# Optimization experiments

Measured on AMD Instinct MI355X. Metric: run time of the kernel, lower is better.

The kernel has to match this reference:

```python
import jax, jax.numpy as jnp
import numpy as np

KS = 3
K2 = KS * KS
PAD = 1


def conv2d(x, w, b=None, stride=1, pad=0):
    out = jax.lax.conv_general_dilated(
        x, w, (stride, stride), [(pad, pad), (pad, pad)],
        dimension_numbers=("NCHW", "OIHW", "NCHW"))
    if b is not None:
        out = out + b[None, :, None, None]
    return out


def setup_inputs() -> dict:
    key = jax.random.key(0)
    ks = jax.random.split(key, 11)
    B, C, H, W = 4, 64, 128, 128
    s = 0.05  # weight scale keeps offsets in a sane range
    return {
        "x":      jax.random.normal(ks[0], (B, C, H, W), jnp.float32),
        "ref":    jax.random.normal(ks[1], (B, C, H, W), jnp.float32),
        "w_cd":   jax.random.normal(ks[2], (C, 2 * C, 1, 1), jnp.float32) * s,
        "b_cd":   jax.random.normal(ks[3], (C,), jnp.float32) * s,
        "w_p":    jax.random.normal(ks[4], (2 * K2, C, 3, 3), jnp.float32) * s,
        "b_p":    jax.random.normal(ks[5], (2 * K2,), jnp.float32) * s,
        "w_m":    jax.random.normal(ks[6], (K2, C, 3, 3), jnp.float32) * s,
        "b_m":    jax.random.normal(ks[7], (K2,), jnp.float32) * s,
        "w_c":    jax.random.normal(ks[8], (K2 * C, C, 3, 3), jnp.float32) * s,
        "b_c":    jax.random.normal(ks[9], (K2 * C,), jnp.float32) * s,
        "w_conv": jax.random.normal(ks[10], (C, C, 3, 3), jnp.float32) * s,
    }


def _deform_forward(x, ref, w_cd, b_cd, w_p, b_p, w_m, b_m, w_c, b_c, w_conv):
    B, C, H, W = x.shape
    dt = x.dtype

    # offset / modulation / color nets on fused input
    fused = conv2d(jnp.concatenate([x, ref], axis=1), w_cd, b_cd)          # [B,C,H,W]
    off = conv2d(fused, w_p, b_p, pad=1)                                    # [B,2K2,H,W]
    mod = jax.nn.sigmoid(conv2d(fused, w_m, b_m, pad=1))                    # [B,K2,H,W]
    col = jnp.tanh(conv2d(fused, w_c, b_c, pad=1))                          # [B,K2*C,H,W]

    # zero-pad input; sampling grid carries the +padding shift (arange starts at 1)
    xp = jnp.pad(x, ((0, 0), (0, 0), (PAD, PAD), (PAD, PAD)))
    Hp, Wp = H + 2 * PAD, W + 2 * PAD

    gx = jnp.broadcast_to(jnp.arange(1, H + 1, dtype=dt)[:, None], (H, W))
    gy = jnp.broadcast_to(jnp.arange(1, W + 1, dtype=dt)[None, :], (H, W))
    r = (KS - 1) // 2
    cx, cy = jnp.meshgrid(jnp.arange(-r, r + 1, dtype=dt),
                          jnp.arange(-r, r + 1, dtype=dt), indexing="ij")
    px = gx[None, None] + off[:, :K2] + cx.ravel()[None, :, None, None]     # [B,K2,H,W]
    py = gy[None, None] + off[:, K2:] + cy.ravel()[None, :, None, None]

    # integer neighbors (detached, like torch .detach().floor())
    fx = jax.lax.stop_gradient(jnp.floor(px))
    fy = jax.lax.stop_gradient(jnp.floor(py))
    q_ltx = jnp.clip(fx, 0, Hp - 1); q_lty = jnp.clip(fy, 0, Wp - 1)
    q_rbx = jnp.clip(fx + 1, 0, Hp - 1); q_rby = jnp.clip(fy + 1, 0, Wp - 1)

    # clamped sampling locations for weights
    sx = jnp.clip(px, 0, Hp - 1)
    sy = jnp.clip(py, 0, Wp - 1)
    g_lt = (1 + (q_ltx - sx)) * (1 + (q_lty - sy))
    g_rb = (1 - (q_rbx - sx)) * (1 - (q_rby - sy))
    g_lb = (1 + (q_ltx - sx)) * (1 - (q_rby - sy))
    g_rt = (1 - (q_rbx - sx)) * (1 + (q_lty - sy))

    xf = xp.reshape(B, C, Hp * Wp)

    def gather(qx, qy):
        idx = (qx.astype(jnp.int32) * Wp + qy.astype(jnp.int32)).reshape(B, -1)
        out = jax.vmap(lambda m, i: m[:, i])(xf, idx)                       # [B,C,K2*H*W]
        return out.reshape(B, C, K2, H, W)

    pos = (g_lt[:, None] * gather(q_ltx, q_lty)
           + g_rb[:, None] * gather(q_rbx, q_rby)
           + g_lb[:, None] * gather(q_ltx, q_rby)
           + g_rt[:, None] * gather(q_rbx, q_lty))                          # [B,C,K2,H,W]

    inp = col.reshape(B, C, K2, H, W) + pos                                 # color deform
    inp = inp * mod[:, None]                                                # modulation

    # [B,C,kx,ky,H,W] -> [B,C,H,kx,W,ky] -> [B,C,H*ks,W*ks]
    io = inp.reshape(B, C, KS, KS, H, W).transpose(0, 1, 4, 2, 5, 3)
    io = io.reshape(B, C, H * KS, W * KS)
    return conv2d(io, w_conv, None, stride=KS)                              # [B,outc,H,W]


def reference(x, ref, w_cd, b_cd, w_p, b_p, w_m, b_m, w_c, b_c, w_conv):
    return _deform_forward(x, ref, w_cd, b_cd, w_p, b_p, w_m, b_m, w_c, b_c, w_conv)
```

## Files before the change

### kernel.cpp

```cpp
#include <hip/hip_runtime.h>
#include <hip/hip_bf16.h>
#include <math.h>

typedef short s16x8 __attribute__((ext_vector_type(8)));
typedef float f32x4 __attribute__((ext_vector_type(4)));

__device__ inline ushort f2bf(float f) {
  unsigned u = __float_as_uint(f);
  u = (u + 0x7FFF + ((u >> 16) & 1)) >> 16;
  return (ushort)u;
}
__device__ inline float bf2f(ushort u) {
  return __uint_as_float(((unsigned)u) << 16);
}
__device__ inline unsigned pkbf(float a, float b) {
  __hip_bfloat162 h = __float22bfloat162_rn(make_float2(a, b));
  return *(unsigned*)&h;
}
__device__ inline float fast_tanh(float v) {
  float e = __builtin_amdgcn_exp2f(v * 2.8853900817779268f);
  return 1.f - 2.f * __builtin_amdgcn_rcpf(e + 1.f);
}
__device__ inline float fast_sigmoid(float v) {
  float e = __builtin_amdgcn_exp2f(v * -1.4426950408889634f);
  return __builtin_amdgcn_rcpf(1.f + e);
}

__global__ __launch_bounds__(256) void k_merge(
    const float* __restrict__ wp, const float* __restrict__ bp,
    const float* __restrict__ wm, const float* __restrict__ bm,
    const float* __restrict__ wc, const float* __restrict__ bc,
    const float* __restrict__ wconv,
    ushort* __restrict__ Wpk, float* __restrict__ Bc, ushort* __restrict__ W2pk) {
  int i = blockIdx.x * 256 + threadIdx.x;
  if (i < 368640) {
    int e = i & 7, lane = (i >> 3) & 63, mi = (i >> 9) & 3, ocq = (i >> 11) & 1;
    int hi = i >> 12;
    int ks = hi % 18, og = hi / 18;
    int g = og * 128 + ocq * 64 + mi * 16 + (lane & 15);
    int ci = ((ks & 1) << 5) + ((lane >> 4) << 3) + e;
    int kk = ks >> 1;
    int col = ci * 9 + kk;
    float v = 0.f;
    if (g < 18)       v = wp[g * 576 + col];
    else if (g < 27)  v = wm[(g - 18) * 576 + col];
    else if (g >= 64) {
      int j = g - 64;
      int cc = (j & 63) * 9 + (j >> 6);
      v = wc[cc * 576 + col];
    }
    Wpk[i] = f2bf(v);
  }
  if (i < 36864) {
    int e = i & 7, lane = (i >> 3) & 63, mi = (i >> 9) & 3, ks = i >> 11;
    int o = mi * 16 + (lane & 15);
    int p = (ks << 5) + ((lane >> 4) << 3) + e;
    int kk2 = p >> 6, c = p & 63;
    W2pk[i] = f2bf(wconv[o * 576 + c * 9 + kk2]);
  }
  if (i < 640) {
    float bv = 0.f;
    if (i < 18)       bv = bp[i];
    else if (i < 27)  bv = bm[i - 18];
    else if (i >= 64) {
      int j = i - 64;
      bv = bc[(j & 63) * 9 + (j >> 6)];
    }
    Bc[i] = bv;
  }
}

__global__ __launch_bounds__(256) void k_fused(
    const float* __restrict__ x, const float* __restrict__ ref,
    const float* __restrict__ wcd, const float* __restrict__ bcd,
    ushort* __restrict__ fusedt) {
  __shared__ float sw[128 * 64];
  __shared__ float sb[64];
  for (int i = threadIdx.x; i < 128 * 64; i += 256) {
    int ci = i >> 6, o = i & 63;
    sw[i] = wcd[o * 128 + ci];
  }
  if (threadIdx.x < 64) sb[threadIdx.x] = bcd[threadIdx.x];
  __syncthreads();

  const int t = threadIdx.x;
  const int pxi = t & 63, oq = t >> 6;
  const int pix = blockIdx.x * 64 + pxi;
  const int b = pix >> 14, hw = pix & 16383;
  const float* xb = x   + ((size_t)b * 64 << 14) + hw;
  const float* rb = ref + ((size_t)b * 64 << 14) + hw;

  float4 acc[4];
  #pragma unroll
  for (int q = 0; q < 4; q++)
    acc[q] = *(const float4*)&sb[oq * 16 + 4 * q];

  for (int ci = 0; ci < 64; ci++) {
    float v = xb[(size_t)ci << 14];
    const float4* wr = (const float4*)&sw[ci * 64 + oq * 16];
    #pragma unroll
    for (int q = 0; q < 4; q++) {
      float4 w4 = wr[q];
      acc[q].x += w4.x * v; acc[q].y += w4.y * v;
      acc[q].z += w4.z * v; acc[q].w += w4.w * v;
    }
  }
  for (int ci = 0; ci < 64; ci++) {
    float v = rb[(size_t)ci << 14];
    const float4* wr = (const float4*)&sw[(64 + ci) * 64 + oq * 16];
    #pragma unroll
    for (int q = 0; q < 4; q++) {
      float4 w4 = wr[q];
      acc[q].x += w4.x * v; acc[q].y += w4.y * v;
      acc[q].z += w4.z * v; acc[q].w += w4.w * v;
    }
  }
  uint4 o0, o1;
  o0.x = pkbf(acc[0].x, acc[0].y); o0.y = pkbf(acc[0].z, acc[0].w);
  o0.z = pkbf(acc[1].x, acc[1].y); o0.w = pkbf(acc[1].z, acc[1].w);
  o1.x = pkbf(acc[2].x, acc[2].y); o1.y = pkbf(acc[2].z, acc[2].w);
  o1.z = pkbf(acc[3].x, acc[3].y); o1.w = pkbf(acc[3].z, acc[3].w);
  ushort* fb = fusedt + ((size_t)pix << 6) + oq * 16;
  *(uint4*)fb       = o0;
  *(uint4*)(fb + 8) = o1;
}

__global__ __launch_bounds__(256) void k_xt(
    const float* __restrict__ x, ushort* __restrict__ xtb) {
  __shared__ float sx[64][65];
  const int t = threadIdx.x;
  const int b = blockIdx.x >> 8, hw0 = (blockIdx.x & 255) << 6;
  for (int i = t; i < 4096; i += 256) {
    int c = i >> 6, hwi = i & 63;
    sx[c][hwi] = x[((size_t)(b * 64 + c) << 14) + hw0 + hwi];
  }
  __syncthreads();
  for (int i = t * 2; i < 4096; i += 512) {
    int hwi = i >> 6, c = i & 63;
    unsigned pk = pkbf(sx[c][hwi], sx[c + 1][hwi]);
    *(unsigned*)(xtb + (((size_t)b << 14) + hw0 + hwi) * 64 + c) = pk;
  }
}

__global__ __launch_bounds__(256) void k_all(
    const ushort* __restrict__ Wpk, const ushort* __restrict__ fusedt,
    const float* __restrict__ Bc, const ushort* __restrict__ xtb,
    const ushort* __restrict__ W2pk, float* __restrict__ out) {
  __shared__ __align__(16) ushort sF[3 * 66 * 64];
  __shared__ __align__(16) ushort colT[64 * 64];
  __shared__ float homT[64 * 27];
  const int t = threadIdx.x;
  const int lane = t & 63, wv = t >> 6;
  const int rowid = blockIdx.x;
  const int b = rowid >> 8;
  const int rem = rowid & 255;
  const int h = rem >> 1, hf = rem & 1;
  const int w0 = hf << 6;
  const int hw0 = (h << 7) + w0;

  for (int idx = t; idx < 1584; idx += 256) {
    int p = idx >> 3, j = idx & 7;
    int row = p / 66, w1 = p - row * 66;
    int gh = h + row - 1, gw = w0 + w1 - 1;
    uint4 v = make_uint4(0u, 0u, 0u, 0u);
    if (gh >= 0 && gh < 128 && (unsigned)gw < 128u)
      v = *(const uint4*)(fusedt + ((size_t)((b << 14) + (gh << 7) + gw) << 6) + j * 8);
    int slot = (j + w1) & 7;
    *(uint4*)(sF + (p << 6) + slot * 8) = v;
  }
  __syncthreads();

  const int pxq = wv & 1, rowq = wv >> 1;
  const int nif = lane & 15, kb = lane >> 4, quad = lane >> 4;

  if (rowq == 0) {
    f32x4 acc[2][2];
    #pragma unroll
    for (int mi = 0; mi < 2; mi++)
      #pragma unroll
      for (int ni = 0; ni < 2; ni++) acc[mi][ni] = (f32x4){0.f, 0.f, 0.f, 0.f};
    #pragma unroll 2
    for (int ks = 0; ks < 18; ks++) {
      const int kk = ks >> 1, half = ks & 1;
      const int dr = kk / 3, dc = kk - dr * 3;
      const ushort* wp8 = Wpk + ((size_t)(ks << 12)) + (lane << 3);
      s16x8 af[2], bfr[2];
      #pragma unroll
      for (int mi = 0; mi < 2; mi++)
        af[mi] = *(const s16x8*)(wp8 + (mi << 9));
      const int gci = half * 4 + kb;
      #pragma unroll
      for (int ni = 0; ni < 2; ni++) {
        int r = (pxq << 5) + ni * 16 + nif;
        int w1 = r + dc;
        int slot = (gci + w1) & 7;
        bfr[ni] = *(const s16x8*)(sF + ((dr * 66 + w1) << 6) + slot * 8);
      }
      #pragma unroll
      for (int mi = 0; mi < 2; mi++)
        #pragma unroll
        for (int ni = 0; ni < 2; ni++)
          acc[mi][ni] = __builtin_amdgcn_mfma_f32_16x16x32_bf16(af[mi], bfr[ni], acc[mi][ni], 0, 0, 0);
    }
    #pragma unroll
    for (int mi = 0; mi < 2; mi++) {
      #pragma unroll
      for (int ni = 0; ni < 2; ni++) {
        int px = (pxq << 5) + ni * 16 + nif;
        #pragma unroll
        for (int r = 0; r < 4; r++) {
          int g = mi * 16 + (quad << 2) + r;
          float v = acc[mi][ni][r] + Bc[g];
          if (g < 18)       homT[px * 27 + g] = v;
          else if (g < 27)  homT[px * 27 + g] = fast_sigmoid(v);
        }
      }
    }
  }

  const int cq = t >> 6, pxl = t & 63, c0 = cq << 4;
  const int ww = w0 + pxl;
  const ushort* xb = xtb + ((size_t)b << 20);

  f32x4 aco[2][2];
  #pragma unroll
  for (int mi = 0; mi < 2; mi++)
    #pragma unroll
    for (int ni = 0; ni < 2; ni++) aco[mi][ni] = (f32x4){0.f, 0.f, 0.f, 0.f};

  #pragma unroll 1
  for (int k = 0; k < 9; k++) {
    const int q = 1 + k, og = q >> 1, ocq = q & 1;
    f32x4 acc[2][2];
    #pragma unroll
    for (int mi = 0; mi < 2; mi++)
      #pragma unroll
      for (int ni = 0; ni < 2; ni++) acc[mi][ni] = (f32x4){0.f, 0.f, 0.f, 0.f};
    #pragma unroll 2
    for (int ks = 0; ks < 18; ks++) {
      const int kk = ks >> 1, half = ks & 1;
      const int dr = kk / 3, dc = kk - dr * 3;
      const ushort* wp8 = Wpk + ((size_t)((((og * 18 + ks) << 1) + ocq) << 11)) + (lane << 3);
      s16x8 af[2], bfr[2];
      #pragma unroll
      for (int mi = 0; mi < 2; mi++)
        af[mi] = *(const s16x8*)(wp8 + (((rowq << 1) + mi) << 9));
      const int gci = half * 4 + kb;
      #pragma unroll
      for (int ni = 0; ni < 2; ni++) {
        int r = (pxq << 5) + ni * 16 + nif;
        int w1 = r + dc;
        int slot = (gci + w1) & 7;
        bfr[ni] = *(const s16x8*)(sF + ((dr * 66 + w1) << 6) + slot * 8);
      }
      #pragma unroll
      for (int mi = 0; mi < 2; mi++)
        #pragma unroll
        for (int ni = 0; ni < 2; ni++)
          acc[mi][ni] = __builtin_amdgcn_mfma_f32_16x16x32_bf16(af[mi], bfr[ni], acc[mi][ni], 0, 0, 0);
    }
    __syncthreads();

    #pragma unroll
    for (int mi = 0; mi < 2; mi++) {
      #pragma unroll
      for (int ni = 0; ni < 2; ni++) {
        int px = (pxq << 5) + ni * 16 + nif;
        int c = (rowq << 5) + mi * 16 + (quad << 2);
        float4 b4 = *(const float4*)(Bc + 64 + (k << 6) + c);
        ushort v4[4];
        v4[0] = f2bf(fast_tanh(acc[mi][ni][0] + b4.x));
        v4[1] = f2bf(fast_tanh(acc[mi][ni][1] + b4.y));
        v4[2] = f2bf(fast_tanh(acc[mi][ni][2] + b4.z));
        v4[3] = f2bf(fast_tanh(acc[mi][ni][3] + b4.w));
        int slot = ((c >> 3) + px) & 7;
        *(uint2*)(colT + (px << 6) + slot * 8 + (c & 7)) = *(uint2*)v4;
      }
    }
    __syncthreads();

    {
      float ox = homT[pxl * 27 + k];
      float oy = homT[pxl * 27 + 9 + k];
      float mk = homT[pxl * 27 + 18 + k];
      float px_ = (float)(h + k / 3) + ox;
      float py_ = (float)(ww + k % 3) + oy;
      float fx = floorf(px_), fy = floorf(py_);
      float qltx = fminf(fmaxf(fx, 0.f), 129.f);
      float qlty = fminf(fmaxf(fy, 0.f), 129.f);
      float qrbx = fminf(fmaxf(fx + 1.f, 0.f), 129.f);
      float qrby = fminf(fmaxf(fy + 1.f, 0.f), 129.f);
      float sx = fminf(fmaxf(px_, 0.f), 129.f);
      float sy = fminf(fmaxf(py_, 0.f), 129.f);
      float ax = 1.f + qltx - sx, bx = 1.f - qrbx + sx;
      float ay = 1.f + qlty - sy, by = 1.f - qrby + sy;
      int iltx = (int)qltx, ilty = (int)qlty, irbx = (int)qrbx, irby = (int)qrby;
      bool vltx = (iltx >= 1) && (iltx <= 128);
      bool vlty = (ilty >= 1) && (ilty <= 128);
      bool vrbx = (irbx >= 1) && (irbx <= 128);
      bool vrby = (irby >= 1) && (irby <= 128);
      float wl[4];
      int   ofs[4];
      wl[0] = (vltx && vlty) ? ax * ay : 0.f;
      wl[1] = (vrbx && vrby) ? bx * by : 0.f;
      wl[2] = (vltx && vrby) ? ax * by : 0.f;
      wl[3] = (vrbx && vlty) ? bx * ay : 0.f;
      ofs[0] = (vltx && vlty) ? ((iltx - 1) << 7) + (ilty - 1) : 0;
      ofs[1] = (vrbx && vrby) ? ((irbx - 1) << 7) + (irby - 1) : 0;
      ofs[2] = (vltx && vrby) ? ((iltx - 1) << 7) + (irby - 1) : 0;
      ofs[3] = (vrbx && vlty) ? ((irbx - 1) << 7) + (ilty - 1) : 0;

      float pos[16];
      #pragma unroll
      for (int j = 0; j < 16; j++) pos[j] = 0.f;
      #pragma unroll
      for (int corner = 0; corner < 4; corner++) {
        const ushort* p = xb + ((size_t)ofs[corner] << 6) + c0;
        float wgt = wl[corner];
        ushort tmp[16];
        *(uint4*)(tmp)     = *(const uint4*)(p);
        *(uint4*)(tmp + 8) = *(const uint4*)(p + 8);
        #pragma unroll
        for (int j = 0; j < 16; j++) pos[j] += wgt * bf2f(tmp[j]);
      }
      #pragma unroll
      for (int q2 = 0; q2 < 2; q2++) {
        int chunk = (cq << 1) + q2;
        int slot = (chunk + pxl) & 7;
        ushort* cp = colT + (pxl << 6) + slot * 8;
        ushort ct[8];
        *(uint4*)ct = *(const uint4*)cp;
        #pragma unroll
        for (int j = 0; j < 8; j++)
          ct[j] = f2bf((bf2f(ct[j]) + pos[q2 * 8 + j]) * mk);
        *(uint4*)cp = *(uint4*)ct;
      }
    }
    __syncthreads();

    #pragma unroll
    for (int khalf = 0; khalf < 2; khalf++) {
      int ks2 = (k << 1) + khalf;
      s16x8 af[2], bfr[2];
      #pragma unroll
      for (int mi = 0; mi < 2; mi++)
        af[mi] = *(const s16x8*)(W2pk + ((((ks2 << 2) + (rowq << 1) + mi) << 6) + lane) * 8);
      const int g0 = (khalf << 2) + kb;
      #pragma unroll
      for (int ni = 0; ni < 2; ni++) {
        int r = (pxq << 5) + ni * 16 + nif;
        int slot = (g0 + r) & 7;
        bfr[ni] = *(const s16x8*)(colT + (r << 6) + slot * 8);
      }
      #pragma unroll
      for (int mi = 0; mi < 2; mi++)
        #pragma unroll
        for (int ni = 0; ni < 2; ni++)
          aco[mi][ni] = __builtin_amdgcn_mfma_f32_16x16x32_bf16(af[mi], bfr[ni], aco[mi][ni], 0, 0, 0);
    }
  }

  #pragma unroll
  for (int mi = 0; mi < 2; mi++) {
    #pragma unroll
    for (int ni = 0; ni < 2; ni++) {
      int hwp = hw0 + (pxq << 5) + ni * 16 + nif;
      #pragma unroll
      for (int r = 0; r < 4; r++) {
        int o = (rowq << 5) + mi * 16 + (quad << 2) + r;
        out[(((size_t)b * 64 + o) << 14) + hwp] = aco[mi][ni][r];
      }
    }
  }
}

extern "C" void kernel_launch(void* const* d_in, const int* in_sizes, int n_in,
                              void* d_out, int out_size, void* d_ws, size_t ws_size,
                              hipStream_t stream) {
  const float* x     = (const float*)d_in[0];
  const float* ref   = (const float*)d_in[1];
  const float* wcd   = (const float*)d_in[2];
  const float* bcd   = (const float*)d_in[3];
  const float* wp    = (const float*)d_in[4];
  const float* bp    = (const float*)d_in[5];
  const float* wm    = (const float*)d_in[6];
  const float* bm    = (const float*)d_in[7];
  const float* wc    = (const float*)d_in[8];
  const float* bc    = (const float*)d_in[9];
  const float* wconv = (const float*)d_in[10];
  float* out = (float*)d_out;

  char* w8 = (char*)d_ws;
  ushort* Wpk     = (ushort*)(w8 + 0);
  float*  Bc      = (float*)(w8 + 737280);
  ushort* W2pk    = (ushort*)(w8 + 739840);
  ushort* fusedt  = (ushort*)(w8 + 813568);
  ushort* xtb     = (ushort*)(w8 + 9202176);

  k_merge <<<1440, 256, 0, stream>>>(wp, bp, wm, bm, wc, bc, wconv, Wpk, Bc, W2pk);
  k_fused <<<1024, 256, 0, stream>>>(x, ref, wcd, bcd, fusedt);
  k_xt    <<<1024, 256, 0, stream>>>(x, xtb);
  k_all   <<<1024, 256, 0, stream>>>(Wpk, fusedt, Bc, xtb, W2pk, out);
}
```

Before: 238.9 us.

## Merge x transpose into fused conv, double-buffer colT, split offset GEMM across waves

Folds the bf16 transpose of x into the 1x1 fused-conv kernel so x is read from global memory once and reused from shared memory, which also removes one launch. In the main kernel the colT tile is double-buffered so the color-net tanh store no longer needs its own barrier. The offset/modulation GEMM is now split across all four waves instead of two, and LDS offsets are precomputed and bf16 unpacking simplified. Launch bounds request three blocks per SM, and the larger shared-memory footprint and extra precomputed offsets add register and occupancy pressure.

```diff
diff --git a/kernel.cpp b/kernel.cpp
--- a/kernel.cpp
+++ b/kernel.cpp
@@ -17,6 +17,8 @@
   __hip_bfloat162 h = __float22bfloat162_rn(make_float2(a, b));
   return *(unsigned*)&h;
 }
+__device__ inline float bflo(unsigned u) { return __uint_as_float(u << 16); }
+__device__ inline float bfhi(unsigned u) { return __uint_as_float(u & 0xffff0000u); }
 __device__ inline float fast_tanh(float v) {
   float e = __builtin_amdgcn_exp2f(v * 2.8853900817779268f);
   return 1.f - 2.f * __builtin_amdgcn_rcpf(e + 1.f);
@@ -73,22 +75,32 @@
 __global__ __launch_bounds__(256) void k_fused(
     const float* __restrict__ x, const float* __restrict__ ref,
     const float* __restrict__ wcd, const float* __restrict__ bcd,
-    ushort* __restrict__ fusedt) {
+    ushort* __restrict__ fusedt, ushort* __restrict__ xtb) {
   __shared__ float sw[128 * 64];
+  __shared__ float sx[64][65];
   __shared__ float sb[64];
-  for (int i = threadIdx.x; i < 128 * 64; i += 256) {
+  const int t = threadIdx.x;
+  for (int i = t; i < 128 * 64; i += 256) {
     int ci = i >> 6, o = i & 63;
     sw[i] = wcd[o * 128 + ci];
   }
-  if (threadIdx.x < 64) sb[threadIdx.x] = bcd[threadIdx.x];
+  if (t < 64) sb[t] = bcd[t];
+  const int b = blockIdx.x >> 8, hw0 = (blockIdx.x & 255) << 6;
+  for (int i = t; i < 4096; i += 256) {
+    int c = i >> 6, hwi = i & 63;
+    sx[c][hwi] = x[((size_t)((b << 6) + c) << 14) + hw0 + hwi];
+  }
   __syncthreads();
 
-  const int t = threadIdx.x;
+  for (int i = t * 2; i < 4096; i += 512) {
+    int hwi = i >> 6, c = i & 63;
+    unsigned pk = pkbf(sx[c][hwi], sx[c + 1][hwi]);
+    *(unsigned*)(xtb + (((size_t)b << 14) + hw0 + hwi) * 64 + c) = pk;
+  }
+
   const int pxi = t & 63, oq = t >> 6;
   const int pix = blockIdx.x * 64 + pxi;
-  const int b = pix >> 14, hw = pix & 16383;
-  const float* xb = x   + ((size_t)b * 64 << 14) + hw;
-  const float* rb = ref + ((size_t)b * 64 << 14) + hw;
+  const float* rb = ref + (((size_t)b << 6) << 14) + hw0 + pxi;
 
   float4 acc[4];
   #pragma unroll
@@ -96,7 +108,7 @@
     acc[q] = *(const float4*)&sb[oq * 16 + 4 * q];
 
   for (int ci = 0; ci < 64; ci++) {
-    float v = xb[(size_t)ci << 14];
+    float v = sx[ci][pxi];
     const float4* wr = (const float4*)&sw[ci * 64 + oq * 16];
     #pragma unroll
     for (int q = 0; q < 4; q++) {
@@ -125,29 +137,12 @@
   *(uint4*)(fb + 8) = o1;
 }
 
-__global__ __launch_bounds__(256) void k_xt(
-    const float* __restrict__ x, ushort* __restrict__ xtb) {
-  __shared__ float sx[64][65];
-  const int t = threadIdx.x;
-  const int b = blockIdx.x >> 8, hw0 = (blockIdx.x & 255) << 6;
-  for (int i = t; i < 4096; i += 256) {
-    int c = i >> 6, hwi = i & 63;
-    sx[c][hwi] = x[((size_t)(b * 64 + c) << 14) + hw0 + hwi];
-  }
-  __syncthreads();
-  for (int i = t * 2; i < 4096; i += 512) {
-    int hwi = i >> 6, c = i & 63;
-    unsigned pk = pkbf(sx[c][hwi], sx[c + 1][hwi]);
-    *(unsigned*)(xtb + (((size_t)b << 14) + hw0 + hwi) * 64 + c) = pk;
-  }
-}
-
-__global__ __launch_bounds__(256) void k_all(
+__global__ __launch_bounds__(256, 3) void k_all(
     const ushort* __restrict__ Wpk, const ushort* __restrict__ fusedt,
     const float* __restrict__ Bc, const ushort* __restrict__ xtb,
     const ushort* __restrict__ W2pk, float* __restrict__ out) {
   __shared__ __align__(16) ushort sF[3 * 66 * 64];
-  __shared__ __align__(16) ushort colT[64 * 64];
+  __shared__ __align__(16) ushort colT[2 * 64 * 64];
   __shared__ float homT[64 * 27];
   const int t = threadIdx.x;
   const int lane = t & 63, wv = t >> 6;
@@ -168,59 +163,70 @@
     int slot = (j + w1) & 7;
     *(uint4*)(sF + (p << 6) + slot * 8) = v;
   }
-  __syncthreads();
 
   const int pxq = wv & 1, rowq = wv >> 1;
   const int nif = lane & 15, kb = lane >> 4, quad = lane >> 4;
-
-  if (rowq == 0) {
-    f32x4 acc[2][2];
-    #pragma unroll
-    for (int mi = 0; mi < 2; mi++)
-      #pragma unroll
-      for (int ni = 0; ni < 2; ni++) acc[mi][ni] = (f32x4){0.f, 0.f, 0.f, 0.f};
-    #pragma unroll 2
+  const int wlaneoff = lane << 3;
+  const int rfq = __builtin_amdgcn_readfirstlane(rowq);
+  const int rowel9  = rfq << 9;
+  const int rowel10 = rfq << 10;
+
+  int sfo[18][2];
+  #pragma unroll
+  for (int ks = 0; ks < 18; ks++) {
+    const int kk = ks >> 1, half = ks & 1;
+    const int dr = kk / 3, dc = kk - dr * 3;
+    const int gci = half * 4 + kb;
+    #pragma unroll
+    for (int ni = 0; ni < 2; ni++) {
+      const int r = (pxq << 5) + ni * 16 + nif;
+      const int w1 = r + dc;
+      sfo[ks][ni] = ((dr * 66 + w1) << 6) + (((gci + w1) & 7) << 3);
+    }
+  }
+  int cto[2][2];
+  #pragma unroll
+  for (int khalf = 0; khalf < 2; khalf++) {
+    const int g0 = (khalf << 2) + kb;
+    #pragma unroll
+    for (int ni = 0; ni < 2; ni++) {
+      const int r = (pxq << 5) + ni * 16 + nif;
+      cto[khalf][ni] = (r << 6) + (((g0 + r) & 7) << 3);
+    }
+  }
+
+  __syncthreads();
+
+  {
+    f32x4 acc[2];
+    acc[0] = (f32x4){0.f, 0.f, 0.f, 0.f};
+    acc[1] = (f32x4){0.f, 0.f, 0.f, 0.f};
+    #pragma unroll
     for (int ks = 0; ks < 18; ks++) {
-      const int kk = ks >> 1, half = ks & 1;
-      const int dr = kk / 3, dc = kk - dr * 3;
-      const ushort* wp8 = Wpk + ((size_t)(ks << 12)) + (lane << 3);
-      s16x8 af[2], bfr[2];
-      #pragma unroll
-      for (int mi = 0; mi < 2; mi++)
-        af[mi] = *(const s16x8*)(wp8 + (mi << 9));
-      const int gci = half * 4 + kb;
-      #pragma unroll
-      for (int ni = 0; ni < 2; ni++) {
-        int r = (pxq << 5) + ni * 16 + nif;
-        int w1 = r + dc;
-        int slot = (gci + w1) & 7;
-        bfr[ni] = *(const s16x8*)(sF + ((dr * 66 + w1) << 6) + slot * 8);
+      s16x8 af = *(const s16x8*)(Wpk + (ks << 12) + rowel9 + wlaneoff);
+      s16x8 b0 = *(const s16x8*)(sF + sfo[ks][0]);
+      s16x8 b1 = *(const s16x8*)(sF + sfo[ks][1]);
+      acc[0] = __builtin_amdgcn_mfma_f32_16x16x32_bf16(af, b0, acc[0], 0, 0, 0);
+      acc[1] = __builtin_amdgcn_mfma_f32_16x16x32_bf16(af, b1, acc[1], 0, 0, 0);
+    }
+    const float4 b4 = *(const float4*)(Bc + (rowq << 4) + (quad << 2));
+    const float bb[4] = {b4.x, b4.y, b4.z, b4.w};
+    #pragma unroll
+    for (int ni = 0; ni < 2; ni++) {
+      const int px = (pxq << 5) + ni * 16 + nif;
+      #pragma unroll
+      for (int r = 0; r < 4; r++) {
+        const int g = (rowq << 4) + (quad << 2) + r;
+        float v = acc[ni][r] + bb[r];
+        if (g < 18)       homT[px * 27 + g] = v;
+        else if (g < 27)  homT[px * 27 + g] = fast_sigmoid(v);
       }
-      #pragma unroll
-      for (int mi = 0; mi < 2; mi++)
-        #pragma unroll
-        for (int ni = 0; ni < 2; ni++)
-          acc[mi][ni] = __builtin_amdgcn_mfma_f32_16x16x32_bf16(af[mi], bfr[ni], acc[mi][ni], 0, 0, 0);
-    }
-    #pragma unroll
-    for (int mi = 0; mi < 2; mi++) {
-      #pragma unroll
-      for (int ni = 0; ni < 2; ni++) {
-        int px = (pxq << 5) + ni * 16 + nif;
-        #pragma unroll
-        for (int r = 0; r < 4; r++) {
-          int g = mi * 16 + (quad << 2) + r;
-          float v = acc[mi][ni][r] + Bc[g];
-          if (g < 18)       homT[px * 27 + g] = v;
-          else if (g < 27)  homT[px * 27 + g] = fast_sigmoid(v);
-        }
-      }
-    }
-  }
-
-  const int cq = t >> 6, pxl = t & 63, c0 = cq << 4;
-  const int ww = w0 + pxl;
-  const ushort* xb = xtb + ((size_t)b << 20);
+    }
+  }
+
+  const int c0 = wv << 4;
+  const int ww = w0 + lane;
+  const ushort* xbc = xtb + ((size_t)b << 20) + c0;
 
   f32x4 aco[2][2];
   #pragma unroll
@@ -230,61 +236,52 @@
 
   #pragma unroll 1
   for (int k = 0; k < 9; k++) {
+    ushort* ctk = colT + ((k & 1) << 12);
+
     const int q = 1 + k, og = q >> 1, ocq = q & 1;
+    const ushort* wb = Wpk + ((size_t)(((og * 36) + ocq) << 11)) + rowel10 + wlaneoff;
     f32x4 acc[2][2];
     #pragma unroll
     for (int mi = 0; mi < 2; mi++)
       #pragma unroll
       for (int ni = 0; ni < 2; ni++) acc[mi][ni] = (f32x4){0.f, 0.f, 0.f, 0.f};
-    #pragma unroll 2
+    #pragma unroll
     for (int ks = 0; ks < 18; ks++) {
-      const int kk = ks >> 1, half = ks & 1;
-      const int dr = kk / 3, dc = kk - dr * 3;
-      const ushort* wp8 = Wpk + ((size_t)((((og * 18 + ks) << 1) + ocq) << 11)) + (lane << 3);
-      s16x8 af[2], bfr[2];
-      #pragma unroll
-      for (int mi = 0; mi < 2; mi++)
-        af[mi] = *(const s16x8*)(wp8 + (((rowq << 1) + mi) << 9));
-      const int gci = half * 4 + kb;
+      const ushort* wp8 = wb + (ks << 12);
+      s16x8 af0 = *(const s16x8*)(wp8);
+      s16x8 af1 = *(const s16x8*)(wp8 + 512);
+      s16x8 b0 = *(const s16x8*)(sF + sfo[ks][0]);
+      s16x8 b1 = *(const s16x8*)(sF + sfo[ks][1]);
+      acc[0][0] = __builtin_amdgcn_mfma_f32_16x16x32_bf16(af0, b0, acc[0][0], 0, 0, 0);
+      acc[0][1] = __builtin_amdgcn_mfma_f32_16x16x32_bf16(af0, b1, acc[0][1], 0, 0, 0);
+      acc[1][0] = __builtin_amdgcn_mfma_f32_16x16x32_bf16(af1, b0, acc[1][0], 0, 0, 0);
+      acc[1][1] = __builtin_amdgcn_mfma_f32_16x16x32_bf16(af1, b1, acc[1][1], 0, 0, 0);
+    }
+
+    #pragma unroll
+    for (int mi = 0; mi < 2; mi++) {
+      const int c = (rowq << 5) + mi * 16 + (quad << 2);
+      const float4 b4 = *(const float4*)(Bc + 64 + (k << 6) + c);
       #pragma unroll
       for (int ni = 0; ni < 2; ni++) {
-        int r = (pxq << 5) + ni * 16 + nif;
-        int w1 = r + dc;
-        int slot = (gci + w1) & 7;
-        bfr[ni] = *(const s16x8*)(sF + ((dr * 66 + w1) << 6) + slot * 8);
+        const int px = (pxq << 5) + ni * 16 + nif;
+        uint2 pk2;
+        pk2.x = pkbf(fast_tanh(acc[mi][ni][0] + b4.x), fast_tanh(acc[mi][ni][1] + b4.y));
+        pk2.y = pkbf(fast_tanh(acc[mi][ni][2] + b4.z), fast_tanh(acc[mi][ni][3] + b4.w));
+        const int slot = ((c >> 3) + px) & 7;
+        *(uint2*)(ctk + (px << 6) + slot * 8 + (c & 7)) = pk2;
       }
-      #pragma unroll
-      for (int mi = 0; mi < 2; mi++)
-        #pragma unroll
-        for (int ni = 0; ni < 2; ni++)
-          acc[mi][ni] = __builtin_amdgcn_mfma_f32_16x16x32_bf16(af[mi], bfr[ni], acc[mi][ni], 0, 0, 0);
     }
     __syncthreads();
 
-    #pragma unroll
-    for (int mi = 0; mi < 2; mi++) {
-      #pragma unroll
-      for (int ni = 0; ni < 2; ni++) {
-        int px = (pxq << 5) + ni * 16 + nif;
-        int c = (rowq << 5) + mi * 16 + (quad << 2);
-        float4 b4 = *(const float4*)(Bc + 64 + (k << 6) + c);
-        ushort v4[4];
-        v4[0] = f2bf(fast_tanh(acc[mi][ni][0] + b4.x));
-        v4[1] = f2bf(fast_tanh(acc[mi][ni][1] + b4.y));
-        v4[2] = f2bf(fast_tanh(acc[mi][ni][2] + b4.z));
-        v4[3] = f2bf(fast_tanh(acc[mi][ni][3] + b4.w));
-        int slot = ((c >> 3) + px) & 7;
-        *(uint2*)(colT + (px << 6) + slot * 8 + (c & 7)) = *(uint2*)v4;
-      }
-    }
-    __syncthreads();
-
     {
-      float ox = homT[pxl * 27 + k];
-      float oy = homT[pxl * 27 + 9 + k];
-      float mk = homT[pxl * 27 + 18 + k];
-      float px_ = (float)(h + k / 3) + ox;
-      float py_ = (float)(ww + k % 3) + oy;
+      const int hb = lane * 27;
+      float ox = homT[hb + k];
+      float oy = homT[hb + 9 + k];
+      float mk = homT[hb + 18 + k];
+      const int kdr = k / 3, kdc = k - kdr * 3;
+      float px_ = (float)(h + kdr) + ox;
+      float py_ = (float)(ww + kdc) + oy;
       float fx = floorf(px_), fy = floorf(py_);
       float qltx = fminf(fmaxf(fx, 0.f), 129.f);
       float qlty = fminf(fmaxf(fy, 0.f), 129.f);
@@ -315,48 +312,55 @@
       for (int j = 0; j < 16; j++) pos[j] = 0.f;
       #pragma unroll
       for (int corner = 0; corner < 4; corner++) {
-        const ushort* p = xb + ((size_t)ofs[corner] << 6) + c0;
+        const ushort* p = xbc + ((size_t)ofs[corner] << 6);
+        uint4 A  = *(const uint4*)(p);
+        uint4 Bv = *(const uint4*)(p + 8);
         float wgt = wl[corner];
-        ushort tmp[16];
-        *(uint4*)(tmp)     = *(const uint4*)(p);
-        *(uint4*)(tmp + 8) = *(const uint4*)(p + 8);
-        #pragma unroll
-        for (int j = 0; j < 16; j++) pos[j] += wgt * bf2f(tmp[j]);
+        pos[0]  += wgt * bflo(A.x);  pos[1]  += wgt * bfhi(A.x);
+        pos[2]  += wgt * bflo(A.y);  pos[3]  += wgt * bfhi(A.y);
+        pos[4]  += wgt * bflo(A.z);  pos[5]  += wgt * bfhi(A.z);
+        pos[6]  += wgt * bflo(A.w);  pos[7]  += wgt * bfhi(A.w);
+        pos[8]  += wgt * bflo(Bv.x); pos[9]  += wgt * bfhi(Bv.x);
+        pos[10] += wgt * bflo(Bv.y); pos[11] += wgt * bfhi(Bv.y);
+        pos[12] += wgt * bflo(Bv.z); pos[13] += wgt * bfhi(Bv.z);
+        pos[14] += wgt * bflo(Bv.w); pos[15] += wgt * bfhi(Bv.w);
       }
       #pragma unroll
       for (int q2 = 0; q2 < 2; q2++) {
-        int chunk = (cq << 1) + q2;
-        int slot = (chunk + pxl) & 7;
-        ushort* cp = colT + (pxl << 6) + slot * 8;
-        ushort ct[8];
-        *(uint4*)ct = *(const uint4*)cp;
-        #pragma unroll
-        for (int j = 0; j < 8; j++)
-          ct[j] = f2bf((bf2f(ct[j]) + pos[q2 * 8 + j]) * mk);
-        *(uint4*)cp = *(uint4*)ct;
+        const int chunk = (wv << 1) + q2;
+        const int slot = (chunk + lane) & 7;
+        ushort* cp = ctk + (lane << 6) + slot * 8;
+        uint4 cw = *(const uint4*)cp;
+        float f0 = bflo(cw.x) + pos[q2 * 8 + 0];
+        float f1 = bfhi(cw.x) + pos[q2 * 8 + 1];
+        float f2 = bflo(cw.y) + pos[q2 * 8 + 2];
+        float f3 = bfhi(cw.y) + pos[q2 * 8 + 3];
+        float f4 = bflo(cw.z) + pos[q2 * 8 + 4];
+        float f5 = bfhi(cw.z) + pos[q2 * 8 + 5];
+        float f6 = bflo(cw.w) + pos[q2 * 8 + 6];
+        float f7 = bfhi(cw.w) + pos[q2 * 8 + 7];
+        uint4 ow;
+        ow.x = pkbf(f0 * mk, f1 * mk);
+        ow.y = pkbf(f2 * mk, f3 * mk);
+        ow.z = pkbf(f4 * mk, f5 * mk);
+        ow.w = pkbf(f6 * mk, f7 * mk);
+        *(uint4*)cp = ow;
       }
     }
     __syncthreads();
 
     #pragma unroll
     for (int khalf = 0; khalf < 2; khalf++) {
-      int ks2 = (k << 1) + khalf;
-      s16x8 af[2], bfr[2];
-      #pragma unroll
-      for (int mi = 0; mi < 2; mi++)
-        af[mi] = *(const s16x8*)(W2pk + ((((ks2 << 2) + (rowq << 1) + mi) << 6) + lane) * 8);
-      const int g0 = (khalf << 2) + kb;
-      #pragma unroll
-      for (int ni = 0; ni < 2; ni++) {
-        int r = (pxq << 5) + ni * 16 + nif;
-        int slot = (g0 + r) & 7;
-        bfr[ni] = *(const s16x8*)(colT + (r << 6) + slot * 8);
-      }
-      #pragma unroll
-      for (int mi = 0; mi < 2; mi++)
-        #pragma unroll
-        for (int ni = 0; ni < 2; ni++)
-          aco[mi][ni] = __builtin_amdgcn_mfma_f32_16x16x32_bf16(af[mi], bfr[ni], aco[mi][ni], 0, 0, 0);
+      const int ks2 = (k << 1) + khalf;
+      const ushort* w2 = W2pk + (ks2 << 11) + rowel10 + wlaneoff;
+      s16x8 af0 = *(const s16x8*)(w2);
+      s16x8 af1 = *(const s16x8*)(w2 + 512);
+      s16x8 b0 = *(const s16x8*)(ctk + cto[khalf][0]);
+      s16x8 b1 = *(const s16x8*)(ctk + cto[khalf][1]);
+      aco[0][0] = __builtin_amdgcn_mfma_f32_16x16x32_bf16(af0, b0, aco[0][0], 0, 0, 0);
+      aco[0][1] = __builtin_amdgcn_mfma_f32_16x16x32_bf16(af0, b1, aco[0][1], 0, 0, 0);
+      aco[1][0] = __builtin_amdgcn_mfma_f32_16x16x32_bf16(af1, b0, aco[1][0], 0, 0, 0);
+      aco[1][1] = __builtin_amdgcn_mfma_f32_16x16x32_bf16(af1, b1, aco[1][1], 0, 0, 0);
     }
   }
 
@@ -398,7 +402,6 @@
   ushort* xtb     = (ushort*)(w8 + 9202176);
 
   k_merge <<<1440, 256, 0, stream>>>(wp, bp, wm, bm, wc, bc, wconv, Wpk, Bc, W2pk);
-  k_fused <<<1024, 256, 0, stream>>>(x, ref, wcd, bcd, fusedt);
-  k_xt    <<<1024, 256, 0, stream>>>(x, xtb);
+  k_fused <<<1024, 256, 0, stream>>>(x, ref, wcd, bcd, fusedt, xtb);
   k_all   <<<1024, 256, 0, stream>>>(Wpk, fusedt, Bc, xtb, W2pk, out);
 }
```

Measured after the change: 275.0 us. +15.1%, slower.

## Merge weight packing, transpose and 1x1 conv into one MFMA kernel

Applied to the files above, without the earlier changes.

Combines the three preprocessing kernels into one launch. Extra blocks do the weight packing, and the main blocks load x once, write the bf16 transpose and compute the 1x1 fused conv with bf16 MFMA instead of scalar FP32 FMAs. This removes two launches and a second read of x, and uses matrix cores for the channel-mixing conv. In exchange, the fused conv now runs with bf16 inputs, which lowers its precision, and LDS use per block goes up.

```diff
diff --git a/kernel.cpp b/kernel.cpp
--- a/kernel.cpp
+++ b/kernel.cpp
@@ -26,119 +26,143 @@
   return __builtin_amdgcn_rcpf(1.f + e);
 }
 
-__global__ __launch_bounds__(256) void k_merge(
+__global__ __launch_bounds__(256) void k_fused(
+    const float* __restrict__ x, const float* __restrict__ ref,
+    const float* __restrict__ wcd, const float* __restrict__ bcd,
     const float* __restrict__ wp, const float* __restrict__ bp,
     const float* __restrict__ wm, const float* __restrict__ bm,
     const float* __restrict__ wc, const float* __restrict__ bc,
     const float* __restrict__ wconv,
+    ushort* __restrict__ fusedt, ushort* __restrict__ xtb,
     ushort* __restrict__ Wpk, float* __restrict__ Bc, ushort* __restrict__ W2pk) {
-  int i = blockIdx.x * 256 + threadIdx.x;
-  if (i < 368640) {
-    int e = i & 7, lane = (i >> 3) & 63, mi = (i >> 9) & 3, ocq = (i >> 11) & 1;
-    int hi = i >> 12;
-    int ks = hi % 18, og = hi / 18;
-    int g = og * 128 + ocq * 64 + mi * 16 + (lane & 15);
-    int ci = ((ks & 1) << 5) + ((lane >> 4) << 3) + e;
-    int kk = ks >> 1;
-    int col = ci * 9 + kk;
-    float v = 0.f;
-    if (g < 18)       v = wp[g * 576 + col];
-    else if (g < 27)  v = wm[(g - 18) * 576 + col];
-    else if (g >= 64) {
-      int j = g - 64;
-      int cc = (j & 63) * 9 + (j >> 6);
-      v = wc[cc * 576 + col];
-    }
-    Wpk[i] = f2bf(v);
-  }
-  if (i < 36864) {
-    int e = i & 7, lane = (i >> 3) & 63, mi = (i >> 9) & 3, ks = i >> 11;
-    int o = mi * 16 + (lane & 15);
-    int p = (ks << 5) + ((lane >> 4) << 3) + e;
-    int kk2 = p >> 6, c = p & 63;
-    W2pk[i] = f2bf(wconv[o * 576 + c * 9 + kk2]);
-  }
-  if (i < 640) {
-    float bv = 0.f;
-    if (i < 18)       bv = bp[i];
-    else if (i < 27)  bv = bm[i - 18];
-    else if (i >= 64) {
-      int j = i - 64;
-      bv = bc[(j & 63) * 9 + (j >> 6)];
-    }
-    Bc[i] = bv;
-  }
-}
-
-__global__ __launch_bounds__(256) void k_fused(
-    const float* __restrict__ x, const float* __restrict__ ref,
-    const float* __restrict__ wcd, const float* __restrict__ bcd,
-    ushort* __restrict__ fusedt) {
-  __shared__ float sw[128 * 64];
+  __shared__ float sxf[64][68];
+  __shared__ __align__(16) ushort w_lds[64 * 128];
+  __shared__ __align__(16) ushort xt_lds[64 * 128];
   __shared__ float sb[64];
-  for (int i = threadIdx.x; i < 128 * 64; i += 256) {
-    int ci = i >> 6, o = i & 63;
-    sw[i] = wcd[o * 128 + ci];
-  }
-  if (threadIdx.x < 64) sb[threadIdx.x] = bcd[threadIdx.x];
-  __syncthreads();
-
-  const int t = threadIdx.x;
-  const int pxi = t & 63, oq = t >> 6;
-  const int pix = blockIdx.x * 64 + pxi;
-  const int b = pix >> 14, hw = pix & 16383;
-  const float* xb = x   + ((size_t)b * 64 << 14) + hw;
-  const float* rb = ref + ((size_t)b * 64 << 14) + hw;
-
-  float4 acc[4];
-  #pragma unroll
-  for (int q = 0; q < 4; q++)
-    acc[q] = *(const float4*)&sb[oq * 16 + 4 * q];
-
-  for (int ci = 0; ci < 64; ci++) {
-    float v = xb[(size_t)ci << 14];
-    const float4* wr = (const float4*)&sw[ci * 64 + oq * 16];
-    #pragma unroll
-    for (int q = 0; q < 4; q++) {
-      float4 w4 = wr[q];
-      acc[q].x += w4.x * v; acc[q].y += w4.y * v;
-      acc[q].z += w4.z * v; acc[q].w += w4.w * v;
-    }
-  }
-  for (int ci = 0; ci < 64; ci++) {
-    float v = rb[(size_t)ci << 14];
-    const float4* wr = (const float4*)&sw[(64 + ci) * 64 + oq * 16];
-    #pragma unroll
-    for (int q = 0; q < 4; q++) {
-      float4 w4 = wr[q];
-      acc[q].x += w4.x * v; acc[q].y += w4.y * v;
-      acc[q].z += w4.z * v; acc[q].w += w4.w * v;
-    }
-  }
-  uint4 o0, o1;
-  o0.x = pkbf(acc[0].x, acc[0].y); o0.y = pkbf(acc[0].z, acc[0].w);
-  o0.z = pkbf(acc[1].x, acc[1].y); o0.w = pkbf(acc[1].z, acc[1].w);
-  o1.x = pkbf(acc[2].x, acc[2].y); o1.y = pkbf(acc[2].z, acc[2].w);
-  o1.z = pkbf(acc[3].x, acc[3].y); o1.w = pkbf(acc[3].z, acc[3].w);
-  ushort* fb = fusedt + ((size_t)pix << 6) + oq * 16;
-  *(uint4*)fb       = o0;
-  *(uint4*)(fb + 8) = o1;
-}
-
-__global__ __launch_bounds__(256) void k_xt(
-    const float* __restrict__ x, ushort* __restrict__ xtb) {
-  __shared__ float sx[64][65];
+
+  if (blockIdx.x >= 1024) {
+    int i = (blockIdx.x - 1024) * 256 + threadIdx.x;
+    if (i < 368640) {
+      int e = i & 7, lane = (i >> 3) & 63, mi = (i >> 9) & 3, ocq = (i >> 11) & 1;
+      int hi = i >> 12;
+      int ks = hi % 18, og = hi / 18;
+      int g = og * 128 + ocq * 64 + mi * 16 + (lane & 15);
+      int ci = ((ks & 1) << 5) + ((lane >> 4) << 3) + e;
+      int kk = ks >> 1;
+      int col = ci * 9 + kk;
+      float v = 0.f;
+      if (g < 18)       v = wp[g * 576 + col];
+      else if (g < 27)  v = wm[(g - 18) * 576 + col];
+      else if (g >= 64) {
+        int j = g - 64;
+        int cc = (j & 63) * 9 + (j >> 6);
+        v = wc[cc * 576 + col];
+      }
+      Wpk[i] = f2bf(v);
+    }
+    if (i < 36864) {
+      int e = i & 7, lane = (i >> 3) & 63, mi = (i >> 9) & 3, ks = i >> 11;
+      int o = mi * 16 + (lane & 15);
+      int p = (ks << 5) + ((lane >> 4) << 3) + e;
+      int kk2 = p >> 6, c = p & 63;
+      W2pk[i] = f2bf(wconv[o * 576 + c * 9 + kk2]);
+    }
+    if (i < 640) {
+      float bv = 0.f;
+      if (i < 18)       bv = bp[i];
+      else if (i < 27)  bv = bm[i - 18];
+      else if (i >= 64) {
+        int j = i - 64;
+        bv = bc[(j & 63) * 9 + (j >> 6)];
+      }
+      Bc[i] = bv;
+    }
+    return;
+  }
+
   const int t = threadIdx.x;
   const int b = blockIdx.x >> 8, hw0 = (blockIdx.x & 255) << 6;
-  for (int i = t; i < 4096; i += 256) {
-    int c = i >> 6, hwi = i & 63;
-    sx[c][hwi] = x[((size_t)(b * 64 + c) << 14) + hw0 + hwi];
+  if (t < 64) sb[t] = bcd[t];
+
+  #pragma unroll
+  for (int rep = 0; rep < 4; rep++) {
+    int idx = t + (rep << 8);
+    int oc = idx >> 4, g = idx & 15;
+    ushort v8[8];
+    #pragma unroll
+    for (int e = 0; e < 8; e++)
+      v8[e] = f2bf(wcd[oc * 128 + (g << 3) + e]);
+    *(uint4*)(w_lds + oc * 128 + (((g + oc) & 15) << 3)) = *(uint4*)v8;
+  }
+
+  #pragma unroll
+  for (int rep = 0; rep < 4; rep++) {
+    int idx = t + (rep << 8);
+    int ci = idx >> 4, p4 = (idx & 15) << 2;
+    float4 v = *(const float4*)(x + ((size_t)((b << 6) + ci) << 14) + hw0 + p4);
+    *(float4*)&sxf[ci][p4] = v;
   }
   __syncthreads();
-  for (int i = t * 2; i < 4096; i += 512) {
-    int hwi = i >> 6, c = i & 63;
-    unsigned pk = pkbf(sx[c][hwi], sx[c + 1][hwi]);
-    *(unsigned*)(xtb + (((size_t)b << 14) + hw0 + hwi) * 64 + c) = pk;
+
+  #pragma unroll
+  for (int rep = 0; rep < 2; rep++) {
+    int idx = t + (rep << 8);
+    int px = idx >> 3, g = idx & 7;
+    ushort v8[8];
+    #pragma unroll
+    for (int e = 0; e < 8; e++)
+      v8[e] = f2bf(sxf[(g << 3) + e][px]);
+    *(uint4*)(xt_lds + px * 128 + (((g + px) & 15) << 3)) = *(uint4*)v8;
+    *(uint4*)(xtb + (((size_t)b << 14) + hw0 + px) * 64 + (g << 3)) = *(uint4*)v8;
+  }
+  __syncthreads();
+
+  #pragma unroll
+  for (int rep = 0; rep < 4; rep++) {
+    int idx = t + (rep << 8);
+    int ci = idx >> 4, p4 = (idx & 15) << 2;
+    float4 v = *(const float4*)(ref + ((size_t)((b << 6) + ci) << 14) + hw0 + p4);
+    *(float4*)&sxf[ci][p4] = v;
+  }
+  __syncthreads();
+
+  #pragma unroll
+  for (int rep = 0; rep < 2; rep++) {
+    int idx = t + (rep << 8);
+    int px = idx >> 3, g = (idx & 7) + 8;
+    ushort v8[8];
+    #pragma unroll
+    for (int e = 0; e < 8; e++)
+      v8[e] = f2bf(sxf[((g & 7) << 3) + e][px]);
+    *(uint4*)(xt_lds + px * 128 + (((g + px) & 15) << 3)) = *(uint4*)v8;
+  }
+  __syncthreads();
+
+  const int lane = t & 63, wv4 = t >> 6;
+  const int ocl = lane & 15, kb = lane >> 4;
+  const int ocr = (wv4 << 4) + ocl;
+  f32x4 acc[4];
+  #pragma unroll
+  for (int ni = 0; ni < 4; ni++) acc[ni] = (f32x4){0.f, 0.f, 0.f, 0.f};
+  #pragma unroll
+  for (int s = 0; s < 4; s++) {
+    const int gA = (s << 2) + kb;
+    s16x8 af = *(const s16x8*)(w_lds + ocr * 128 + (((gA + ocr) & 15) << 3));
+    #pragma unroll
+    for (int ni = 0; ni < 4; ni++) {
+      const int px = (ni << 4) + ocl;
+      s16x8 bf8 = *(const s16x8*)(xt_lds + px * 128 + (((gA + px) & 15) << 3));
+      acc[ni] = __builtin_amdgcn_mfma_f32_16x16x32_bf16(af, bf8, acc[ni], 0, 0, 0);
+    }
+  }
+  const float4 b4 = *(const float4*)&sb[(wv4 << 4) + (kb << 2)];
+  #pragma unroll
+  for (int ni = 0; ni < 4; ni++) {
+    const int px = (ni << 4) + ocl;
+    uint2 o;
+    o.x = pkbf(acc[ni][0] + b4.x, acc[ni][1] + b4.y);
+    o.y = pkbf(acc[ni][2] + b4.z, acc[ni][3] + b4.w);
+    *(uint2*)(fusedt + (((size_t)(b << 14) + hw0 + px) << 6) + (wv4 << 4) + (kb << 2)) = o;
   }
 }
 
@@ -397,8 +421,7 @@
   ushort* fusedt  = (ushort*)(w8 + 813568);
   ushort* xtb     = (ushort*)(w8 + 9202176);
 
-  k_merge <<<1440, 256, 0, stream>>>(wp, bp, wm, bm, wc, bc, wconv, Wpk, Bc, W2pk);
-  k_fused <<<1024, 256, 0, stream>>>(x, ref, wcd, bcd, fusedt);
-  k_xt    <<<1024, 256, 0, stream>>>(x, xtb);
+  k_fused <<<2464, 256, 0, stream>>>(x, ref, wcd, bcd, wp, bp, wm, bm, wc, bc, wconv,
+                                     fusedt, xtb, Wpk, Bc, W2pk);
   k_all   <<<1024, 256, 0, stream>>>(Wpk, fusedt, Bc, xtb, W2pk, out);
 }
```

After: 198.9 us. -16.8%, faster.
